# Performance work log

Hardware: AMD Instinct MI355X
Metric: run time of the kernel (lower is better)

Reference implementation:

```python
import jax, jax.numpy as jnp
import numpy as np

N_NODES = 50000
N_EDGES = 800000
IN_FEATS = 128
OUT_FEATS = 128


def setup_inputs() -> dict:
    key = jax.random.key(0)
    k1, k2, k3, k4 = jax.random.split(key, 4)
    x = jax.random.normal(k1, (N_NODES, IN_FEATS), dtype=jnp.float32)
    src = jax.random.randint(k2, (N_EDGES,), 0, N_NODES, dtype=jnp.int32)
    dst = jax.random.randint(k3, (N_EDGES,), 0, N_NODES, dtype=jnp.int32)
    # xavier_uniform init for weight [in_feats, out_feats]
    limit = float(np.sqrt(6.0 / (IN_FEATS + OUT_FEATS)))
    weight = jax.random.uniform(k4, (IN_FEATS, OUT_FEATS), dtype=jnp.float32,
                                minval=-limit, maxval=limit)
    bias = jnp.zeros((OUT_FEATS,), dtype=jnp.float32)
    return {"x": x, "src": src, "dst": dst, "weight": weight, "bias": bias}


def reference(x, src, dst, weight, bias):
    # GraphConv, norm='both', no edge_weight (copy_u path), single partition:
    #   x <- x * out_deg^{-1/2}
    #   h[v] = sum_{(u->v) in E} x[u]            (SpMM aggregation)
    #   rst = h @ W                               (GEMM)
    #   rst <- rst * in_deg^{-1/2} + bias
    n = x.shape[0]
    ones = jnp.ones(src.shape[0], dtype=x.dtype)
    deg_out = jax.ops.segment_sum(ones, src, num_segments=n)     # [N]
    deg_out = jnp.maximum(deg_out, 1.0)[:, None]                  # clamp(min=1)
    xn = x * jax.lax.rsqrt(deg_out)                               # left norm
    h = jax.ops.segment_sum(xn[src], dst, num_segments=n)        # [N, in]
    rst = h @ weight                                              # [N, out]
    deg_in = jax.ops.segment_sum(ones, dst, num_segments=n)      # [N]
    deg_in = jnp.maximum(deg_in, 1.0)[:, None]
    rst = rst * jax.lax.rsqrt(deg_in)                             # right norm
    return rst + bias
```

## Files before the change

### kernel.cpp

```cpp
#include <hip/hip_runtime.h>

#define F 128
#define RANGE 12500
#define WT_LD 136

typedef unsigned short ushort_t;
typedef unsigned char uchar_t;
typedef _Float16 half8 __attribute__((ext_vector_type(8)));
typedef float f32x4 __attribute__((ext_vector_type(4)));

__device__ inline float bf_lo(unsigned u) { return __uint_as_float(u << 16); }
__device__ inline float bf_hi(unsigned u) { return __uint_as_float(u & 0xffff0000u); }
__device__ inline ushort_t f2bf(float f) {
    unsigned u = __float_as_uint(f);
    return (ushort_t)((u + 0x7fff + ((u >> 16) & 1)) >> 16);
}

__global__ __launch_bounds__(1024)
void hist_both_kernel(const int* __restrict__ src, const int* __restrict__ dst,
                      ushort_t* __restrict__ part, int E, int S, int SLICE) {
    __shared__ int h[RANGE];
    int b = blockIdx.x, t = threadIdx.x;
    int r = b / S, s = b % S;
    int lo = r * RANGE;
    for (int i = t; i < RANGE; i += 1024) h[i] = 0;
    __syncthreads();
    int e0 = s * SLICE, e1 = min(e0 + SLICE, E);
    int e = e0 + t * 4;
    for (; e + 3 < e1; e += 4096) {
        int4 vs4 = *(const int4*)(src + e);
        int4 vd4 = *(const int4*)(dst + e);
        int vs, vd;
        vs = vs4.x - lo; if ((unsigned)vs < (unsigned)RANGE) atomicAdd(&h[vs], 1);
        vs = vs4.y - lo; if ((unsigned)vs < (unsigned)RANGE) atomicAdd(&h[vs], 1);
        vs = vs4.z - lo; if ((unsigned)vs < (unsigned)RANGE) atomicAdd(&h[vs], 1);
        vs = vs4.w - lo; if ((unsigned)vs < (unsigned)RANGE) atomicAdd(&h[vs], 1);
        vd = vd4.x - lo; if ((unsigned)vd < (unsigned)RANGE) atomicAdd(&h[vd], 0x10000);
        vd = vd4.y - lo; if ((unsigned)vd < (unsigned)RANGE) atomicAdd(&h[vd], 0x10000);
        vd = vd4.z - lo; if ((unsigned)vd < (unsigned)RANGE) atomicAdd(&h[vd], 0x10000);
        vd = vd4.w - lo; if ((unsigned)vd < (unsigned)RANGE) atomicAdd(&h[vd], 0x10000);
    }
    for (; e < e1; ++e) {
        int vs = src[e] - lo;
        int vd = dst[e] - lo;
        if ((unsigned)vs < (unsigned)RANGE) atomicAdd(&h[vs], 1);
        if ((unsigned)vd < (unsigned)RANGE) atomicAdd(&h[vd], 0x10000);
    }
    __syncthreads();
    ushort_t* outp = part + (size_t)b * RANGE;
    for (int i = t; i < RANGE; i += 1024) {
        int hv = h[i];
        outp[i] = (ushort_t)((hv & 0xff) | ((hv >> 8) & 0xff00));
    }
}

__global__ __launch_bounds__(256)
void reduce_all_kernel(const ushort_t* __restrict__ part, uchar_t* __restrict__ pre8,
                       float* __restrict__ inv_out, int* __restrict__ cnt_in,
                       int* __restrict__ psum, int S, int N) {
    int b = blockIdx.x, t = threadIdx.x;
    int v = b * 256 + t;
    int run = 0;
    if (v < N) {
        int r = v / RANGE, vp = v % RANGE;
        const ushort_t* p = part + (size_t)r * S * RANGE + vp;
        uchar_t* q = pre8 + (size_t)r * S * RANGE + vp;
        int sum_s = 0;
        #pragma unroll 8
        for (int s = 0; s < S; ++s) {
            int tv = p[(size_t)s * RANGE];
            sum_s += tv & 0xff;
            q[(size_t)s * RANGE] = (uchar_t)run;
            run += (tv >> 8);
        }
        inv_out[v] = rsqrtf(fmaxf((float)sum_s, 1.0f));
        cnt_in[v] = run;
    }
    int bl = run;
    #pragma unroll
    for (int off = 32; off > 0; off >>= 1) bl += __shfl_down(bl, off);
    __shared__ int ws[4];
    int lane = t & 63, w = t >> 6;
    if (lane == 0) ws[w] = bl;
    __syncthreads();
    if (t == 0) psum[b] = ws[0] + ws[1] + ws[2] + ws[3];
}

__global__ __launch_bounds__(256)
void scan_rows_kernel(const int* __restrict__ cnt_in, const int* __restrict__ psum,
                      int* __restrict__ row_off, int N, int E, int NP) {
    int b = blockIdx.x, t = threadIdx.x;
    int pv = (t < 4 * b && t < NP) ? psum[t] : 0;
    #pragma unroll
    for (int off = 32; off > 0; off >>= 1) pv += __shfl_down(pv, off);
    __shared__ int red[4];
    int lane = t & 63, w = t >> 6;
    if (lane == 0) red[w] = pv;
    if (b == 0 && t == 0) row_off[N] = E;
    __syncthreads();
    int base = red[0] + red[1] + red[2] + red[3];

    int i0 = b * 1024 + t * 4;
    int v[4]; int s = 0;
    #pragma unroll
    for (int j = 0; j < 4; ++j) { int i = i0 + j; v[j] = (i < N) ? cnt_in[i] : 0; s += v[j]; }
    int incl = s;
    #pragma unroll
    for (int off = 1; off < 64; off <<= 1) {
        int u = __shfl_up(incl, off);
        if (lane >= off) incl += u;
    }
    __shared__ int wsum[4];
    if (lane == 63) wsum[w] = incl;
    __syncthreads();
    int wbase = 0;
    #pragma unroll
    for (int j = 0; j < 4; ++j) if (j < w) wbase += wsum[j];
    int run = base + wbase + (incl - s);
    #pragma unroll
    for (int j = 0; j < 4; ++j) {
        int i = i0 + j;
        if (i < N) { row_off[i] = run; run += v[j]; }
    }
}

__global__ __launch_bounds__(1024)
void fill_gemm_kernel(const int* __restrict__ src, const int* __restrict__ dst,
                      const int* __restrict__ row_off, const uchar_t* __restrict__ pre8,
                      ushort_t* __restrict__ csr_src,
                      const float* __restrict__ x, const float* __restrict__ W,
                      const float* __restrict__ inv_out, ushort_t* __restrict__ Y,
                      int E, int S, int SLICE, int N, int FB) {
    __shared__ union {
        int cur[RANGE];
        _Float16 Wt[128 * WT_LD];
    } sm;
    const int t = threadIdx.x;
    const int blk = blockIdx.x;

    if (blk < FB) {
        int r = blk / S, s = blk % S;
        int lo = r * RANGE;
        int hi = min(lo + RANGE, N);
        const uchar_t* pp = pre8 + (size_t)blk * RANGE;
        for (int i = t; i < hi - lo; i += 1024) sm.cur[i] = row_off[lo + i] + pp[i];
        __syncthreads();
        int e0 = s * SLICE, e1 = min(e0 + SLICE, E);
        int e = e0 + t * 4;
        for (; e + 3 < e1; e += 4096) {
            int4 vd4 = *(const int4*)(dst + e);
            int4 vs4 = *(const int4*)(src + e);
            int d;
            d = vd4.x - lo; if ((unsigned)d < (unsigned)(hi - lo)) { int pos = atomicAdd(&sm.cur[d], 1); csr_src[pos] = (ushort_t)vs4.x; }
            d = vd4.y - lo; if ((unsigned)d < (unsigned)(hi - lo)) { int pos = atomicAdd(&sm.cur[d], 1); csr_src[pos] = (ushort_t)vs4.y; }
            d = vd4.z - lo; if ((unsigned)d < (unsigned)(hi - lo)) { int pos = atomicAdd(&sm.cur[d], 1); csr_src[pos] = (ushort_t)vs4.z; }
            d = vd4.w - lo; if ((unsigned)d < (unsigned)(hi - lo)) { int pos = atomicAdd(&sm.cur[d], 1); csr_src[pos] = (ushort_t)vs4.w; }
        }
        for (; e < e1; ++e) {
            int d = dst[e] - lo;
            if ((unsigned)d < (unsigned)(hi - lo)) {
                int pos = atomicAdd(&sm.cur[d], 1);
                csr_src[pos] = (ushort_t)src[e];
            }
        }
        return;
    }

    const int gb = blk - FB;
    for (int i = t; i < 128 * 128; i += 1024) {
        int k = i >> 7, c = i & 127;
        sm.Wt[c * WT_LD + k] = (_Float16)W[i];
    }
    __syncthreads();

    const int wv = t >> 6;
    const int l  = t & 63;
    const int m  = l & 15;
    const int q  = l >> 4;
    const int r0w = gb * 256 + wv * 16;
    const int rowload = min(r0w + m, N - 1);
    const float* xr = x + (size_t)rowload * F;

    f32x4 acc[8] = {};
    #pragma unroll
    for (int k0 = 0; k0 < 128; k0 += 32) {
        const int kk = k0 + q * 8;
        float4 xa = *(const float4*)(xr + kk);
        float4 xb = *(const float4*)(xr + kk + 4);
        half8 a;
        a[0] = (_Float16)xa.x; a[1] = (_Float16)xa.y;
        a[2] = (_Float16)xa.z; a[3] = (_Float16)xa.w;
        a[4] = (_Float16)xb.x; a[5] = (_Float16)xb.y;
        a[6] = (_Float16)xb.z; a[7] = (_Float16)xb.w;
        #pragma unroll
        for (int ct = 0; ct < 8; ++ct) {
            half8 bfr = *(const half8*)&sm.Wt[(ct * 16 + m) * WT_LD + kk];
            acc[ct] = __builtin_amdgcn_mfma_f32_16x16x32_f16(a, bfr, acc[ct], 0, 0, 0);
        }
    }

    float sc[4]; int rvalid[4];
    #pragma unroll
    for (int reg = 0; reg < 4; ++reg) {
        int rr = r0w + q * 4 + reg;
        rvalid[reg] = rr < N;
        sc[reg] = inv_out[min(rr, N - 1)];
    }
    #pragma unroll
    for (int ct = 0; ct < 8; ++ct) {
        #pragma unroll
        for (int reg = 0; reg < 4; ++reg) {
            if (rvalid[reg]) {
                int rr = r0w + q * 4 + reg;
                Y[(size_t)rr * F + ct * 16 + m] = f2bf(acc[ct][reg] * sc[reg]);
            }
        }
    }
}

__global__ __launch_bounds__(256)
void gather_kernel(const ushort_t* __restrict__ Y, const ushort_t* __restrict__ csr_src,
                   const int* __restrict__ row_off, const float* __restrict__ bias,
                   float* __restrict__ out, int N) {
    int v = blockIdx.x * 4 + (threadIdx.x >> 6);
    if (v >= N) return;
    int lane = threadIdx.x & 63;
    int q = lane >> 4;
    int l16 = lane & 15;
    int beg = row_off[v], end = row_off[v + 1];
    float aA[8] = {0,0,0,0,0,0,0,0};
    float aB[8] = {0,0,0,0,0,0,0,0};
    float aC[8] = {0,0,0,0,0,0,0,0};
    float aD[8] = {0,0,0,0,0,0,0,0};
    int j = beg + q;
    for (; j + 12 < end; j += 16) {
        int s0 = csr_src[j];
        int s1 = csr_src[j + 4];
        int s2 = csr_src[j + 8];
        int s3 = csr_src[j + 12];
        uint4 u0 = *(const uint4*)(Y + (size_t)s0 * F + l16 * 8);
        uint4 u1 = *(const uint4*)(Y + (size_t)s1 * F + l16 * 8);
        uint4 u2 = *(const uint4*)(Y + (size_t)s2 * F + l16 * 8);
        uint4 u3 = *(const uint4*)(Y + (size_t)s3 * F + l16 * 8);
        aA[0] += bf_lo(u0.x); aA[1] += bf_hi(u0.x);
        aA[2] += bf_lo(u0.y); aA[3] += bf_hi(u0.y);
        aA[4] += bf_lo(u0.z); aA[5] += bf_hi(u0.z);
        aA[6] += bf_lo(u0.w); aA[7] += bf_hi(u0.w);
        aB[0] += bf_lo(u1.x); aB[1] += bf_hi(u1.x);
        aB[2] += bf_lo(u1.y); aB[3] += bf_hi(u1.y);
        aB[4] += bf_lo(u1.z); aB[5] += bf_hi(u1.z);
        aB[6] += bf_lo(u1.w); aB[7] += bf_hi(u1.w);
        aC[0] += bf_lo(u2.x); aC[1] += bf_hi(u2.x);
        aC[2] += bf_lo(u2.y); aC[3] += bf_hi(u2.y);
        aC[4] += bf_lo(u2.z); aC[5] += bf_hi(u2.z);
        aC[6] += bf_lo(u2.w); aC[7] += bf_hi(u2.w);
        aD[0] += bf_lo(u3.x); aD[1] += bf_hi(u3.x);
        aD[2] += bf_lo(u3.y); aD[3] += bf_hi(u3.y);
        aD[4] += bf_lo(u3.z); aD[5] += bf_hi(u3.z);
        aD[6] += bf_lo(u3.w); aD[7] += bf_hi(u3.w);
    }
    if (j < end) {
        int s0 = csr_src[j];
        uint4 u0 = *(const uint4*)(Y + (size_t)s0 * F + l16 * 8);
        aA[0] += bf_lo(u0.x); aA[1] += bf_hi(u0.x);
        aA[2] += bf_lo(u0.y); aA[3] += bf_hi(u0.y);
        aA[4] += bf_lo(u0.z); aA[5] += bf_hi(u0.z);
        aA[6] += bf_lo(u0.w); aA[7] += bf_hi(u0.w);
    }
    if (j + 4 < end) {
        int s1 = csr_src[j + 4];
        uint4 u1 = *(const uint4*)(Y + (size_t)s1 * F + l16 * 8);
        aB[0] += bf_lo(u1.x); aB[1] += bf_hi(u1.x);
        aB[2] += bf_lo(u1.y); aB[3] += bf_hi(u1.y);
        aB[4] += bf_lo(u1.z); aB[5] += bf_hi(u1.z);
        aB[6] += bf_lo(u1.w); aB[7] += bf_hi(u1.w);
    }
    if (j + 8 < end) {
        int s2 = csr_src[j + 8];
        uint4 u2 = *(const uint4*)(Y + (size_t)s2 * F + l16 * 8);
        aC[0] += bf_lo(u2.x); aC[1] += bf_hi(u2.x);
        aC[2] += bf_lo(u2.y); aC[3] += bf_hi(u2.y);
        aC[4] += bf_lo(u2.z); aC[5] += bf_hi(u2.z);
        aC[6] += bf_lo(u2.w); aC[7] += bf_hi(u2.w);
    }
    #pragma unroll
    for (int i = 0; i < 8; ++i) {
        float a = (aA[i] + aB[i]) + (aC[i] + aD[i]);
        a += __shfl_xor(a, 16);
        a += __shfl_xor(a, 32);
        aA[i] = a;
    }
    if (q == 0) {
        float invd = rsqrtf(fmaxf((float)(end - beg), 1.0f));
        float4 b0 = *(const float4*)(bias + l16 * 8);
        float4 b1 = *(const float4*)(bias + l16 * 8 + 4);
        float4 o0, o1;
        o0.x = aA[0] * invd + b0.x; o0.y = aA[1] * invd + b0.y;
        o0.z = aA[2] * invd + b0.z; o0.w = aA[3] * invd + b0.w;
        o1.x = aA[4] * invd + b1.x; o1.y = aA[5] * invd + b1.y;
        o1.z = aA[6] * invd + b1.z; o1.w = aA[7] * invd + b1.w;
        *(float4*)(out + (size_t)v * F + l16 * 8) = o0;
        *(float4*)(out + (size_t)v * F + l16 * 8 + 4) = o1;
    }
}

extern "C" void kernel_launch(void* const* d_in, const int* in_sizes, int n_in,
                              void* d_out, int out_size, void* d_ws, size_t ws_size,
                              hipStream_t stream) {
    const float* x    = (const float*)d_in[0];
    const int*   src  = (const int*)d_in[1];
    const int*   dst  = (const int*)d_in[2];
    const float* W    = (const float*)d_in[3];
    const float* bias = (const float*)d_in[4];
    float* out = (float*)d_out;

    const int N = in_sizes[0] / F;
    const int E = in_sizes[1];
    const int NB = (N + 1023) / 1024;
    const int NP = (N + 255) / 256;
    const int R = (N + RANGE - 1) / RANGE;

    size_t fixed_bytes = (size_t)N * 4
                       + (size_t)(N + 1) * 4
                       + (size_t)N * 4
                       + (size_t)NP * 4 + 256
                       + (size_t)E * 2 + 256
                       + (size_t)N * F * 2 + 256;
    int S = 64;
    while (S > 2 && fixed_bytes + (size_t)R * S * RANGE * 3 > ws_size) S >>= 1;
    const int SLICE = (E + S - 1) / S;
    const size_t K = (size_t)R * S * RANGE;

    char* base = (char*)d_ws;
    int*   cnt_in  = (int*)base;
    int*   row_off = cnt_in + N;
    float* inv_out = (float*)(row_off + N + 1);
    int*   psum    = (int*)(inv_out + N);
    size_t o1 = (((size_t)NP * 4 + (size_t)(3 * N + 1) * 4) + 255) & ~(size_t)255;
    ushort_t* csr_src = (ushort_t*)(base + o1);
    size_t o2 = (o1 + (size_t)E * 2 + 255) & ~(size_t)255;
    ushort_t* Y    = (ushort_t*)(base + o2);
    size_t o3 = (o2 + (size_t)N * F * 2 + 255) & ~(size_t)255;
    ushort_t* part = (ushort_t*)(base + o3);
    size_t o4 = (o3 + K * 2 + 255) & ~(size_t)255;
    uchar_t* pre8  = (uchar_t*)(base + o4);

    const int hgrid = R * S;
    const int GB = (N + 255) / 256;

    hist_both_kernel<<<hgrid, 1024, 0, stream>>>(src, dst, part, E, S, SLICE);
    reduce_all_kernel<<<NP, 256, 0, stream>>>(part, pre8, inv_out, cnt_in, psum, S, N);
    scan_rows_kernel<<<NB, 256, 0, stream>>>(cnt_in, psum, row_off, N, E, NP);
    fill_gemm_kernel<<<hgrid + GB, 1024, 0, stream>>>(src, dst, row_off, pre8, csr_src,
                                                      x, W, inv_out, Y, E, S, SLICE, N, hgrid);
    gather_kernel<<<(N + 3) / 4, 256, 0, stream>>>(Y, csr_src, row_off, bias, out, N);
}
```

Baseline: 148.8 us.

## Split GEMM across histogram and fill kernels, move out-degree scaling into gather

The dense X·W GEMM no longer depends on the out-degree normalization, so half of its row blocks now run inside the histogram kernel and the other half inside the CSR fill kernel. This lets tensor-core work overlap both atomic-heavy phases instead of only the fill. To make that possible, the left normalization is applied per edge in the gather kernel, which adds one inv_out load per neighbor and a multiply per accumulated element. It also rounds unscaled values to bf16 before scaling, which changes rounding slightly.

Measured after the change: 152.0 us. 1.02x slower.

```diff
diff --git a/kernel.cpp b/kernel.cpp
--- a/kernel.cpp
+++ b/kernel.cpp
@@ -16,14 +16,68 @@
     return (ushort_t)((u + 0x7fff + ((u >> 16) & 1)) >> 16);
 }
 
+__device__ __forceinline__
+void gemm_body(_Float16* Wt, const float* __restrict__ x, const float* __restrict__ W,
+               ushort_t* __restrict__ Y, int N, int gb) {
+    const int t = threadIdx.x;
+    for (int i = t; i < 128 * 128; i += 1024) {
+        int k = i >> 7, c = i & 127;
+        Wt[c * WT_LD + k] = (_Float16)W[i];
+    }
+    __syncthreads();
+
+    const int wv = t >> 6;
+    const int l  = t & 63;
+    const int m  = l & 15;
+    const int q  = l >> 4;
+    const int r0w = gb * 256 + wv * 16;
+    const int rowload = min(r0w + m, N - 1);
+    const float* xr = x + (size_t)rowload * F;
+
+    f32x4 acc[8] = {};
+    #pragma unroll
+    for (int k0 = 0; k0 < 128; k0 += 32) {
+        const int kk = k0 + q * 8;
+        float4 xa = *(const float4*)(xr + kk);
+        float4 xb = *(const float4*)(xr + kk + 4);
+        half8 a;
+        a[0] = (_Float16)xa.x; a[1] = (_Float16)xa.y;
+        a[2] = (_Float16)xa.z; a[3] = (_Float16)xa.w;
+        a[4] = (_Float16)xb.x; a[5] = (_Float16)xb.y;
+        a[6] = (_Float16)xb.z; a[7] = (_Float16)xb.w;
+        #pragma unroll
+        for (int ct = 0; ct < 8; ++ct) {
+            half8 bfr = *(const half8*)&Wt[(ct * 16 + m) * WT_LD + kk];
+            acc[ct] = __builtin_amdgcn_mfma_f32_16x16x32_f16(a, bfr, acc[ct], 0, 0, 0);
+        }
+    }
+
+    #pragma unroll
+    for (int ct = 0; ct < 8; ++ct) {
+        #pragma unroll
+        for (int reg = 0; reg < 4; ++reg) {
+            int rr = r0w + q * 4 + reg;
+            if (rr < N) Y[(size_t)rr * F + ct * 16 + m] = f2bf(acc[ct][reg]);
+        }
+    }
+}
+
 __global__ __launch_bounds__(1024)
-void hist_both_kernel(const int* __restrict__ src, const int* __restrict__ dst,
-                      ushort_t* __restrict__ part, int E, int S, int SLICE) {
-    __shared__ int h[RANGE];
+void hist_gemm_kernel(const int* __restrict__ src, const int* __restrict__ dst,
+                      ushort_t* __restrict__ part, int E, int S, int SLICE,
+                      const float* __restrict__ x, const float* __restrict__ W,
+                      ushort_t* __restrict__ Y, int N, int HB) {
+    __shared__ union {
+        int h[RANGE];
+        _Float16 Wt[128 * WT_LD];
+    } sm;
     int b = blockIdx.x, t = threadIdx.x;
+
+    if (b >= HB) { gemm_body(sm.Wt, x, W, Y, N, b - HB); return; }
+
     int r = b / S, s = b % S;
     int lo = r * RANGE;
-    for (int i = t; i < RANGE; i += 1024) h[i] = 0;
+    for (int i = t; i < RANGE; i += 1024) sm.h[i] = 0;
     __syncthreads();
     int e0 = s * SLICE, e1 = min(e0 + SLICE, E);
     int e = e0 + t * 4;
@@ -31,25 +85,25 @@
         int4 vs4 = *(const int4*)(src + e);
         int4 vd4 = *(const int4*)(dst + e);
         int vs, vd;
-        vs = vs4.x - lo; if ((unsigned)vs < (unsigned)RANGE) atomicAdd(&h[vs], 1);
-        vs = vs4.y - lo; if ((unsigned)vs < (unsigned)RANGE) atomicAdd(&h[vs], 1);
-        vs = vs4.z - lo; if ((unsigned)vs < (unsigned)RANGE) atomicAdd(&h[vs], 1);
-        vs = vs4.w - lo; if ((unsigned)vs < (unsigned)RANGE) atomicAdd(&h[vs], 1);
-        vd = vd4.x - lo; if ((unsigned)vd < (unsigned)RANGE) atomicAdd(&h[vd], 0x10000);
-        vd = vd4.y - lo; if ((unsigned)vd < (unsigned)RANGE) atomicAdd(&h[vd], 0x10000);
-        vd = vd4.z - lo; if ((unsigned)vd < (unsigned)RANGE) atomicAdd(&h[vd], 0x10000);
-        vd = vd4.w - lo; if ((unsigned)vd < (unsigned)RANGE) atomicAdd(&h[vd], 0x10000);
+        vs = vs4.x - lo; if ((unsigned)vs < (unsigned)RANGE) atomicAdd(&sm.h[vs], 1);
+        vs = vs4.y - lo; if ((unsigned)vs < (unsigned)RANGE) atomicAdd(&sm.h[vs], 1);
+        vs = vs4.z - lo; if ((unsigned)vs < (unsigned)RANGE) atomicAdd(&sm.h[vs], 1);
+        vs = vs4.w - lo; if ((unsigned)vs < (unsigned)RANGE) atomicAdd(&sm.h[vs], 1);
+        vd = vd4.x - lo; if ((unsigned)vd < (unsigned)RANGE) atomicAdd(&sm.h[vd], 0x10000);
+        vd = vd4.y - lo; if ((unsigned)vd < (unsigned)RANGE) atomicAdd(&sm.h[vd], 0x10000);
+        vd = vd4.z - lo; if ((unsigned)vd < (unsigned)RANGE) atomicAdd(&sm.h[vd], 0x10000);
+        vd = vd4.w - lo; if ((unsigned)vd < (unsigned)RANGE) atomicAdd(&sm.h[vd], 0x10000);
     }
     for (; e < e1; ++e) {
         int vs = src[e] - lo;
         int vd = dst[e] - lo;
-        if ((unsigned)vs < (unsigned)RANGE) atomicAdd(&h[vs], 1);
-        if ((unsigned)vd < (unsigned)RANGE) atomicAdd(&h[vd], 0x10000);
+        if ((unsigned)vs < (unsigned)RANGE) atomicAdd(&sm.h[vs], 1);
+        if ((unsigned)vd < (unsigned)RANGE) atomicAdd(&sm.h[vd], 0x10000);
     }
     __syncthreads();
     ushort_t* outp = part + (size_t)b * RANGE;
     for (int i = t; i < RANGE; i += 1024) {
-        int hv = h[i];
+        int hv = sm.h[i];
         outp[i] = (ushort_t)((hv & 0xff) | ((hv >> 8) & 0xff00));
     }
 }
@@ -129,8 +183,8 @@
                       const int* __restrict__ row_off, const uchar_t* __restrict__ pre8,
                       ushort_t* __restrict__ csr_src,
                       const float* __restrict__ x, const float* __restrict__ W,
-                      const float* __restrict__ inv_out, ushort_t* __restrict__ Y,
-                      int E, int S, int SLICE, int N, int FB) {
+                      ushort_t* __restrict__ Y,
+                      int E, int S, int SLICE, int N, int FB, int G1) {
     __shared__ union {
         int cur[RANGE];
         _Float16 Wt[128 * WT_LD];
@@ -138,90 +192,38 @@
     const int t = threadIdx.x;
     const int blk = blockIdx.x;
 
-    if (blk < FB) {
-        int r = blk / S, s = blk % S;
-        int lo = r * RANGE;
-        int hi = min(lo + RANGE, N);
-        const uchar_t* pp = pre8 + (size_t)blk * RANGE;
-        for (int i = t; i < hi - lo; i += 1024) sm.cur[i] = row_off[lo + i] + pp[i];
-        __syncthreads();
-        int e0 = s * SLICE, e1 = min(e0 + SLICE, E);
-        int e = e0 + t * 4;
-        for (; e + 3 < e1; e += 4096) {
-            int4 vd4 = *(const int4*)(dst + e);
-            int4 vs4 = *(const int4*)(src + e);
-            int d;
-            d = vd4.x - lo; if ((unsigned)d < (unsigned)(hi - lo)) { int pos = atomicAdd(&sm.cur[d], 1); csr_src[pos] = (ushort_t)vs4.x; }
-            d = vd4.y - lo; if ((unsigned)d < (unsigned)(hi - lo)) { int pos = atomicAdd(&sm.cur[d], 1); csr_src[pos] = (ushort_t)vs4.y; }
-            d = vd4.z - lo; if ((unsigned)d < (unsigned)(hi - lo)) { int pos = atomicAdd(&sm.cur[d], 1); csr_src[pos] = (ushort_t)vs4.z; }
-            d = vd4.w - lo; if ((unsigned)d < (unsigned)(hi - lo)) { int pos = atomicAdd(&sm.cur[d], 1); csr_src[pos] = (ushort_t)vs4.w; }
-        }
-        for (; e < e1; ++e) {
-            int d = dst[e] - lo;
-            if ((unsigned)d < (unsigned)(hi - lo)) {
-                int pos = atomicAdd(&sm.cur[d], 1);
-                csr_src[pos] = (ushort_t)src[e];
-            }
-        }
-        return;
-    }
-
-    const int gb = blk - FB;
-    for (int i = t; i < 128 * 128; i += 1024) {
-        int k = i >> 7, c = i & 127;
-        sm.Wt[c * WT_LD + k] = (_Float16)W[i];
-    }
-    __syncthreads();
-
-    const int wv = t >> 6;
-    const int l  = t & 63;
-    const int m  = l & 15;
-    const int q  = l >> 4;
-    const int r0w = gb * 256 + wv * 16;
-    const int rowload = min(r0w + m, N - 1);
-    const float* xr = x + (size_t)rowload * F;
-
-    f32x4 acc[8] = {};
-    #pragma unroll
-    for (int k0 = 0; k0 < 128; k0 += 32) {
-        const int kk = k0 + q * 8;
-        float4 xa = *(const float4*)(xr + kk);
-        float4 xb = *(const float4*)(xr + kk + 4);
-        half8 a;
-        a[0] = (_Float16)xa.x; a[1] = (_Float16)xa.y;
-        a[2] = (_Float16)xa.z; a[3] = (_Float16)xa.w;
-        a[4] = (_Float16)xb.x; a[5] = (_Float16)xb.y;
-        a[6] = (_Float16)xb.z; a[7] = (_Float16)xb.w;
-        #pragma unroll
-        for (int ct = 0; ct < 8; ++ct) {
-            half8 bfr = *(const half8*)&sm.Wt[(ct * 16 + m) * WT_LD + kk];
-            acc[ct] = __builtin_amdgcn_mfma_f32_16x16x32_f16(a, bfr, acc[ct], 0, 0, 0);
-        }
-    }
-
-    float sc[4]; int rvalid[4];
-    #pragma unroll
-    for (int reg = 0; reg < 4; ++reg) {
-        int rr = r0w + q * 4 + reg;
-        rvalid[reg] = rr < N;
-        sc[reg] = inv_out[min(rr, N - 1)];
-    }
-    #pragma unroll
-    for (int ct = 0; ct < 8; ++ct) {
-        #pragma unroll
-        for (int reg = 0; reg < 4; ++reg) {
-            if (rvalid[reg]) {
-                int rr = r0w + q * 4 + reg;
-                Y[(size_t)rr * F + ct * 16 + m] = f2bf(acc[ct][reg] * sc[reg]);
-            }
+    if (blk >= FB) { gemm_body(sm.Wt, x, W, Y, N, G1 + (blk - FB)); return; }
+
+    int r = blk / S, s = blk % S;
+    int lo = r * RANGE;
+    int hi = min(lo + RANGE, N);
+    const uchar_t* pp = pre8 + (size_t)blk * RANGE;
+    for (int i = t; i < hi - lo; i += 1024) sm.cur[i] = row_off[lo + i] + pp[i];
+    __syncthreads();
+    int e0 = s * SLICE, e1 = min(e0 + SLICE, E);
+    int e = e0 + t * 4;
+    for (; e + 3 < e1; e += 4096) {
+        int4 vd4 = *(const int4*)(dst + e);
+        int4 vs4 = *(const int4*)(src + e);
+        int d;
+        d = vd4.x - lo; if ((unsigned)d < (unsigned)(hi - lo)) { int pos = atomicAdd(&sm.cur[d], 1); csr_src[pos] = (ushort_t)vs4.x; }
+        d = vd4.y - lo; if ((unsigned)d < (unsigned)(hi - lo)) { int pos = atomicAdd(&sm.cur[d], 1); csr_src[pos] = (ushort_t)vs4.y; }
+        d = vd4.z - lo; if ((unsigned)d < (unsigned)(hi - lo)) { int pos = atomicAdd(&sm.cur[d], 1); csr_src[pos] = (ushort_t)vs4.z; }
+        d = vd4.w - lo; if ((unsigned)d < (unsigned)(hi - lo)) { int pos = atomicAdd(&sm.cur[d], 1); csr_src[pos] = (ushort_t)vs4.w; }
+    }
+    for (; e < e1; ++e) {
+        int d = dst[e] - lo;
+        if ((unsigned)d < (unsigned)(hi - lo)) {
+            int pos = atomicAdd(&sm.cur[d], 1);
+            csr_src[pos] = (ushort_t)src[e];
         }
     }
 }
 
 __global__ __launch_bounds__(256)
 void gather_kernel(const ushort_t* __restrict__ Y, const ushort_t* __restrict__ csr_src,
-                   const int* __restrict__ row_off, const float* __restrict__ bias,
-                   float* __restrict__ out, int N) {
+                   const int* __restrict__ row_off, const float* __restrict__ inv_out,
+                   const float* __restrict__ bias, float* __restrict__ out, int N) {
     int v = blockIdx.x * 4 + (threadIdx.x >> 6);
     if (v >= N) return;
     int lane = threadIdx.x & 63;
@@ -238,50 +240,57 @@
         int s1 = csr_src[j + 4];
         int s2 = csr_src[j + 8];
         int s3 = csr_src[j + 12];
+        float iv0 = inv_out[s0];
+        float iv1 = inv_out[s1];
+        float iv2 = inv_out[s2];
+        float iv3 = inv_out[s3];
         uint4 u0 = *(const uint4*)(Y + (size_t)s0 * F + l16 * 8);
         uint4 u1 = *(const uint4*)(Y + (size_t)s1 * F + l16 * 8);
         uint4 u2 = *(const uint4*)(Y + (size_t)s2 * F + l16 * 8);
         uint4 u3 = *(const uint4*)(Y + (size_t)s3 * F + l16 * 8);
-        aA[0] += bf_lo(u0.x); aA[1] += bf_hi(u0.x);
-        aA[2] += bf_lo(u0.y); aA[3] += bf_hi(u0.y);
-        aA[4] += bf_lo(u0.z); aA[5] += bf_hi(u0.z);
-        aA[6] += bf_lo(u0.w); aA[7] += bf_hi(u0.w);
-        aB[0] += bf_lo(u1.x); aB[1] += bf_hi(u1.x);
-        aB[2] += bf_lo(u1.y); aB[3] += bf_hi(u1.y);
-        aB[4] += bf_lo(u1.z); aB[5] += bf_hi(u1.z);
-        aB[6] += bf_lo(u1.w); aB[7] += bf_hi(u1.w);
-        aC[0] += bf_lo(u2.x); aC[1] += bf_hi(u2.x);
-        aC[2] += bf_lo(u2.y); aC[3] += bf_hi(u2.y);
-        aC[4] += bf_lo(u2.z); aC[5] += bf_hi(u2.z);
-        aC[6] += bf_lo(u2.w); aC[7] += bf_hi(u2.w);
-        aD[0] += bf_lo(u3.x); aD[1] += bf_hi(u3.x);
-        aD[2] += bf_lo(u3.y); aD[3] += bf_hi(u3.y);
-        aD[4] += bf_lo(u3.z); aD[5] += bf_hi(u3.z);
-        aD[6] += bf_lo(u3.w); aD[7] += bf_hi(u3.w);
+        aA[0] += bf_lo(u0.x) * iv0; aA[1] += bf_hi(u0.x) * iv0;
+        aA[2] += bf_lo(u0.y) * iv0; aA[3] += bf_hi(u0.y) * iv0;
+        aA[4] += bf_lo(u0.z) * iv0; aA[5] += bf_hi(u0.z) * iv0;
+        aA[6] += bf_lo(u0.w) * iv0; aA[7] += bf_hi(u0.w) * iv0;
+        aB[0] += bf_lo(u1.x) * iv1; aB[1] += bf_hi(u1.x) * iv1;
+        aB[2] += bf_lo(u1.y) * iv1; aB[3] += bf_hi(u1.y) * iv1;
+        aB[4] += bf_lo(u1.z) * iv1; aB[5] += bf_hi(u1.z) * iv1;
+        aB[6] += bf_lo(u1.w) * iv1; aB[7] += bf_hi(u1.w) * iv1;
+        aC[0] += bf_lo(u2.x) * iv2; aC[1] += bf_hi(u2.x) * iv2;
+        aC[2] += bf_lo(u2.y) * iv2; aC[3] += bf_hi(u2.y) * iv2;
+        aC[4] += bf_lo(u2.z) * iv2; aC[5] += bf_hi(u2.z) * iv2;
+        aC[6] += bf_lo(u2.w) * iv2; aC[7] += bf_hi(u2.w) * iv2;
+        aD[0] += bf_lo(u3.x) * iv3; aD[1] += bf_hi(u3.x) * iv3;
+        aD[2] += bf_lo(u3.y) * iv3; aD[3] += bf_hi(u3.y) * iv3;
+        aD[4] += bf_lo(u3.z) * iv3; aD[5] += bf_hi(u3.z) * iv3;
+        aD[6] += bf_lo(u3.w) * iv3; aD[7] += bf_hi(u3.w) * iv3;
     }
     if (j < end) {
         int s0 = csr_src[j];
+        float iv0 = inv_out[s0];
         uint4 u0 = *(const uint4*)(Y + (size_t)s0 * F + l16 * 8);
-        aA[0] += bf_lo(u0.x); aA[1] += bf_hi(u0.x);
-        aA[2] += bf_lo(u0.y); aA[3] += bf_hi(u0.y);
-        aA[4] += bf_lo(u0.z); aA[5] += bf_hi(u0.z);
-        aA[6] += bf_lo(u0.w); aA[7] += bf_hi(u0.w);
+        aA[0] += bf_lo(u0.x) * iv0; aA[1] += bf_hi(u0.x) * iv0;
+        aA[2] += bf_lo(u0.y) * iv0; aA[3] += bf_hi(u0.y) * iv0;
+        aA[4] += bf_lo(u0.z) * iv0; aA[5] += bf_hi(u0.z) * iv0;
+        aA[6] += bf_lo(u0.w) * iv0; aA[7] += bf_hi(u0.w) * iv0;
     }
     if (j + 4 < end) {
         int s1 = csr_src[j + 4];
+        float iv1 = inv_out[s1];
         uint4 u1 = *(const uint4*)(Y + (size_t)s1 * F + l16 * 8);
-        aB[0] += bf_lo(u1.x); aB[1] += bf_hi(u1.x);
-        aB[2] += bf_lo(u1.y); aB[3] += bf_hi(u1.y);
-        aB[4] += bf_lo(u1.z); aB[5] += bf_hi(u1.z);
-        aB[6] += bf_lo(u1.w); aB[7] += bf_hi(u1.w);
+        aB[0] += bf_lo(u1.x) * iv1; aB[1] += bf_hi(u1.x) * iv1;
+        aB[2] += bf_lo(u1.y) * iv1; aB[3] += bf_hi(u1.y) * iv1;
+        aB[4] += bf_lo(u1.z) * iv1; aB[5] += bf_hi(u1.z) * iv1;
+        aB[6] += bf_lo(u1.w) * iv1; aB[7] += bf_hi(u1.w) * iv1;
     }
     if (j + 8 < end) {
         int s2 = csr_src[j + 8];
+        float iv2 = inv_out[s2];
         uint4 u2 = *(const uint4*)(Y + (size_t)s2 * F + l16 * 8);
-        aC[0] += bf_lo(u2.x); aC[1] += bf_hi(u2.x);
-        aC[2] += bf_lo(u2.y); aC[3] += bf_hi(u2.y);
-        aC[4] += bf_lo(u2.z); aC[5] += bf_hi(u2.z);
-        aC[6] += bf_lo(u2.w); aC[7] += bf_hi(u2.w);
+        aC[0] += bf_lo(u2.x) * iv2; aC[1] += bf_hi(u2.x) * iv2;
+        aC[2] += bf_lo(u2.y) * iv2; aC[3] += bf_hi(u2.y) * iv2;
+        aC[4] += bf_lo(u2.z) * iv2; aC[5] += bf_hi(u2.z) * iv2;
+        aC[6] += bf_lo(u2.w) * iv2; aC[7] += bf_hi(u2.w) * iv2;
     }
     #pragma unroll
     for (int i = 0; i < 8; ++i) {
@@ -347,11 +356,15 @@
 
     const int hgrid = R * S;
     const int GB = (N + 255) / 256;
-
-    hist_both_kernel<<<hgrid, 1024, 0, stream>>>(src, dst, part, E, S, SLICE);
+    const int G1 = GB / 2;
+    const int G2 = GB - G1;
+
+    hist_gemm_kernel<<<hgrid + G1, 1024, 0, stream>>>(src, dst, part, E, S, SLICE,
+                                                      x, W, Y, N, hgrid);
     reduce_all_kernel<<<NP, 256, 0, stream>>>(part, pre8, inv_out, cnt_in, psum, S, N);
     scan_rows_kernel<<<NB, 256, 0, stream>>>(cnt_in, psum, row_off, N, E, NP);
-    fill_gemm_kernel<<<hgrid + GB, 1024, 0, stream>>>(src, dst, row_off, pre8, csr_src,
-                                                      x, W, inv_out, Y, E, S, SLICE, N, hgrid);
-    gather_kernel<<<(N + 3) / 4, 256, 0, stream>>>(Y, csr_src, row_off, bias, out, N);
-}
+    fill_gemm_kernel<<<hgrid + G2, 1024, 0, stream>>>(src, dst, row_off, pre8, csr_src,
+                                                      x, W, Y, E, S, SLICE, N, hgrid, G1);
+    gather_kernel<<<(N + 3) / 4, 256, 0, stream>>>(Y, csr_src, row_off, inv_out,
+                                                   bias, out, N);
+}
```

## Pack histogram counters as 8-bit pairs to cover wider node ranges

Applied to the files above, without the earlier changes.

The histogram kernel now packs two nodes' src/dst 8-bit counters into each 32-bit shared word, so one block covers 25000 nodes instead of 12500. Each block handles a smaller edge slice (128 slices), and the raw packed words are stored without repacking. The reduce kernel emits prefix bytes only every other slice to match the coarser 64-slice fill pass. This halves the number of range passes over the edge list in the histogram stage. The risk is that 8-bit per-slice counters overflow for high-degree nodes, and the workspace-size fallback that used to shrink the slice count is gone.

Result: slower. 152.8 us (+2.7%).

```diff
diff --git a/kernel.cpp b/kernel.cpp
--- a/kernel.cpp
+++ b/kernel.cpp
@@ -1,7 +1,10 @@
 #include <hip/hip_runtime.h>
 
 #define F 128
-#define RANGE 12500
+#define RANGE_F 12500
+#define RANGE_H 25000
+#define S_H 128
+#define S_F 64
 #define WT_LD 136
 
 typedef unsigned short ushort_t;
@@ -18,59 +21,57 @@
 
 __global__ __launch_bounds__(1024)
 void hist_both_kernel(const int* __restrict__ src, const int* __restrict__ dst,
-                      ushort_t* __restrict__ part, int E, int S, int SLICE) {
-    __shared__ int h[RANGE];
+                      ushort_t* __restrict__ part, int E, int SLICE) {
+    __shared__ int h[RANGE_H / 2];
     int b = blockIdx.x, t = threadIdx.x;
-    int r = b / S, s = b % S;
-    int lo = r * RANGE;
-    for (int i = t; i < RANGE; i += 1024) h[i] = 0;
+    int r = b / S_H, s = b % S_H;
+    int lo = r * RANGE_H;
+    for (int i = t; i < RANGE_H / 2; i += 1024) h[i] = 0;
     __syncthreads();
     int e0 = s * SLICE, e1 = min(e0 + SLICE, E);
     int e = e0 + t * 4;
     for (; e + 3 < e1; e += 4096) {
         int4 vs4 = *(const int4*)(src + e);
         int4 vd4 = *(const int4*)(dst + e);
-        int vs, vd;
-        vs = vs4.x - lo; if ((unsigned)vs < (unsigned)RANGE) atomicAdd(&h[vs], 1);
-        vs = vs4.y - lo; if ((unsigned)vs < (unsigned)RANGE) atomicAdd(&h[vs], 1);
-        vs = vs4.z - lo; if ((unsigned)vs < (unsigned)RANGE) atomicAdd(&h[vs], 1);
-        vs = vs4.w - lo; if ((unsigned)vs < (unsigned)RANGE) atomicAdd(&h[vs], 1);
-        vd = vd4.x - lo; if ((unsigned)vd < (unsigned)RANGE) atomicAdd(&h[vd], 0x10000);
-        vd = vd4.y - lo; if ((unsigned)vd < (unsigned)RANGE) atomicAdd(&h[vd], 0x10000);
-        vd = vd4.z - lo; if ((unsigned)vd < (unsigned)RANGE) atomicAdd(&h[vd], 0x10000);
-        vd = vd4.w - lo; if ((unsigned)vd < (unsigned)RANGE) atomicAdd(&h[vd], 0x10000);
+        int v;
+        v = vs4.x - lo; if ((unsigned)v < (unsigned)RANGE_H) atomicAdd(&h[v >> 1], 1 << ((v & 1) * 16));
+        v = vs4.y - lo; if ((unsigned)v < (unsigned)RANGE_H) atomicAdd(&h[v >> 1], 1 << ((v & 1) * 16));
+        v = vs4.z - lo; if ((unsigned)v < (unsigned)RANGE_H) atomicAdd(&h[v >> 1], 1 << ((v & 1) * 16));
+        v = vs4.w - lo; if ((unsigned)v < (unsigned)RANGE_H) atomicAdd(&h[v >> 1], 1 << ((v & 1) * 16));
+        v = vd4.x - lo; if ((unsigned)v < (unsigned)RANGE_H) atomicAdd(&h[v >> 1], 0x100 << ((v & 1) * 16));
+        v = vd4.y - lo; if ((unsigned)v < (unsigned)RANGE_H) atomicAdd(&h[v >> 1], 0x100 << ((v & 1) * 16));
+        v = vd4.z - lo; if ((unsigned)v < (unsigned)RANGE_H) atomicAdd(&h[v >> 1], 0x100 << ((v & 1) * 16));
+        v = vd4.w - lo; if ((unsigned)v < (unsigned)RANGE_H) atomicAdd(&h[v >> 1], 0x100 << ((v & 1) * 16));
     }
     for (; e < e1; ++e) {
         int vs = src[e] - lo;
         int vd = dst[e] - lo;
-        if ((unsigned)vs < (unsigned)RANGE) atomicAdd(&h[vs], 1);
-        if ((unsigned)vd < (unsigned)RANGE) atomicAdd(&h[vd], 0x10000);
-    }
-    __syncthreads();
-    ushort_t* outp = part + (size_t)b * RANGE;
-    for (int i = t; i < RANGE; i += 1024) {
-        int hv = h[i];
-        outp[i] = (ushort_t)((hv & 0xff) | ((hv >> 8) & 0xff00));
-    }
+        if ((unsigned)vs < (unsigned)RANGE_H) atomicAdd(&h[vs >> 1], 1 << ((vs & 1) * 16));
+        if ((unsigned)vd < (unsigned)RANGE_H) atomicAdd(&h[vd >> 1], 0x100 << ((vd & 1) * 16));
+    }
+    __syncthreads();
+    int* outp = (int*)(part + (size_t)b * RANGE_H);
+    for (int i = t; i < RANGE_H / 2; i += 1024) outp[i] = h[i];
 }
 
 __global__ __launch_bounds__(256)
 void reduce_all_kernel(const ushort_t* __restrict__ part, uchar_t* __restrict__ pre8,
                        float* __restrict__ inv_out, int* __restrict__ cnt_in,
-                       int* __restrict__ psum, int S, int N) {
+                       int* __restrict__ psum, int N) {
     int b = blockIdx.x, t = threadIdx.x;
     int v = b * 256 + t;
     int run = 0;
     if (v < N) {
-        int r = v / RANGE, vp = v % RANGE;
-        const ushort_t* p = part + (size_t)r * S * RANGE + vp;
-        uchar_t* q = pre8 + (size_t)r * S * RANGE + vp;
+        int rh = v / RANGE_H, vph = v % RANGE_H;
+        const ushort_t* p = part + (size_t)rh * S_H * RANGE_H + vph;
+        int rf = v / RANGE_F, vpf = v % RANGE_F;
+        uchar_t* q = pre8 + (size_t)rf * S_F * RANGE_F + vpf;
         int sum_s = 0;
         #pragma unroll 8
-        for (int s = 0; s < S; ++s) {
-            int tv = p[(size_t)s * RANGE];
+        for (int s = 0; s < S_H; ++s) {
+            if ((s & 1) == 0) q[(size_t)(s >> 1) * RANGE_F] = (uchar_t)run;
+            int tv = p[(size_t)s * RANGE_H];
             sum_s += tv & 0xff;
-            q[(size_t)s * RANGE] = (uchar_t)run;
             run += (tv >> 8);
         }
         inv_out[v] = rsqrtf(fmaxf((float)sum_s, 1.0f));
@@ -130,19 +131,19 @@
                       ushort_t* __restrict__ csr_src,
                       const float* __restrict__ x, const float* __restrict__ W,
                       const float* __restrict__ inv_out, ushort_t* __restrict__ Y,
-                      int E, int S, int SLICE, int N, int FB) {
+                      int E, int SLICE, int N, int FB) {
     __shared__ union {
-        int cur[RANGE];
+        int cur[RANGE_F];
         _Float16 Wt[128 * WT_LD];
     } sm;
     const int t = threadIdx.x;
     const int blk = blockIdx.x;
 
     if (blk < FB) {
-        int r = blk / S, s = blk % S;
-        int lo = r * RANGE;
-        int hi = min(lo + RANGE, N);
-        const uchar_t* pp = pre8 + (size_t)blk * RANGE;
+        int r = blk / S_F, s = blk % S_F;
+        int lo = r * RANGE_F;
+        int hi = min(lo + RANGE_F, N);
+        const uchar_t* pp = pre8 + (size_t)blk * RANGE_F;
         for (int i = t; i < hi - lo; i += 1024) sm.cur[i] = row_off[lo + i] + pp[i];
         __syncthreads();
         int e0 = s * SLICE, e1 = min(e0 + SLICE, E);
@@ -318,18 +319,13 @@
     const int E = in_sizes[1];
     const int NB = (N + 1023) / 1024;
     const int NP = (N + 255) / 256;
-    const int R = (N + RANGE - 1) / RANGE;
-
-    size_t fixed_bytes = (size_t)N * 4
-                       + (size_t)(N + 1) * 4
-                       + (size_t)N * 4
-                       + (size_t)NP * 4 + 256
-                       + (size_t)E * 2 + 256
-                       + (size_t)N * F * 2 + 256;
-    int S = 64;
-    while (S > 2 && fixed_bytes + (size_t)R * S * RANGE * 3 > ws_size) S >>= 1;
-    const int SLICE = (E + S - 1) / S;
-    const size_t K = (size_t)R * S * RANGE;
+    const int RH = (N + RANGE_H - 1) / RANGE_H;
+    const int RF = (N + RANGE_F - 1) / RANGE_F;
+
+    const int SLICE_H = (((E + S_H - 1) / S_H) + 3) & ~3;
+    const int SLICE_F = 2 * SLICE_H;
+    const size_t KH = (size_t)RH * S_H * RANGE_H;
+    const size_t KF = (size_t)RF * S_F * RANGE_F;
 
     char* base = (char*)d_ws;
     int*   cnt_in  = (int*)base;
@@ -342,16 +338,17 @@
     ushort_t* Y    = (ushort_t*)(base + o2);
     size_t o3 = (o2 + (size_t)N * F * 2 + 255) & ~(size_t)255;
     ushort_t* part = (ushort_t*)(base + o3);
-    size_t o4 = (o3 + K * 2 + 255) & ~(size_t)255;
+    size_t o4 = (o3 + KH * 2 + 255) & ~(size_t)255;
     uchar_t* pre8  = (uchar_t*)(base + o4);
 
-    const int hgrid = R * S;
+    const int hgrid = RH * S_H;
+    const int fgrid = RF * S_F;
     const int GB = (N + 255) / 256;
 
-    hist_both_kernel<<<hgrid, 1024, 0, stream>>>(src, dst, part, E, S, SLICE);
-    reduce_all_kernel<<<NP, 256, 0, stream>>>(part, pre8, inv_out, cnt_in, psum, S, N);
+    hist_both_kernel<<<hgrid, 1024, 0, stream>>>(src, dst, part, E, SLICE_H);
+    reduce_all_kernel<<<NP, 256, 0, stream>>>(part, pre8, inv_out, cnt_in, psum, N);
     scan_rows_kernel<<<NB, 256, 0, stream>>>(cnt_in, psum, row_off, N, E, NP);
-    fill_gemm_kernel<<<hgrid + GB, 1024, 0, stream>>>(src, dst, row_off, pre8, csr_src,
-                                                      x, W, inv_out, Y, E, S, SLICE, N, hgrid);
+    fill_gemm_kernel<<<fgrid + GB, 1024, 0, stream>>>(src, dst, row_off, pre8, csr_src,
+                                                      x, W, inv_out, Y, E, SLICE_F, N, fgrid);
     gather_kernel<<<(N + 3) / 4, 256, 0, stream>>>(Y, csr_src, row_off, bias, out, N);
 }
```
